# Kernel optimization log

Measured on AMD Instinct MI355X. Metric: run time of the kernel, lower is better.

## Reference

```python
import jax, jax.numpy as jnp
import numpy as np

B, C, H, W = 8, 512, 32, 32
N_HEADS = 4
D_K = C // N_HEADS  # 128


def setup_inputs() -> dict:
    key = jax.random.key(0)
    k1, k2, k3, k4, k5 = jax.random.split(key, 5)
    x = jax.random.normal(k1, (B, C, H, W), dtype=jnp.float32)
    # projection: Linear(in_ch, n_heads*d_k*3)
    Wp = jax.random.normal(k2, (C, N_HEADS * D_K * 3), dtype=jnp.float32) * (C ** -0.5)
    bp = jax.random.normal(k3, (N_HEADS * D_K * 3,), dtype=jnp.float32) * 0.01
    # output: Linear(n_heads*d_k, in_ch)
    Wo = jax.random.normal(k4, (N_HEADS * D_K, C), dtype=jnp.float32) * ((N_HEADS * D_K) ** -0.5)
    bo = jax.random.normal(k5, (C,), dtype=jnp.float32) * 0.01
    return {"x": x, "Wp": Wp, "bp": bp, "Wo": Wo, "bo": bo}


def reference(x, Wp, bp, Wo, bo):
    b, c, h, w = x.shape
    scale = D_K ** -0.5
    # [B, C, H, W] -> [B, N, C], N = H*W
    xs = x.reshape(b, c, h * w).transpose(0, 2, 1)
    qkv = (xs @ Wp + bp).reshape(b, h * w, N_HEADS, 3 * D_K)
    q, k, v = jnp.split(qkv, 3, axis=-1)  # each [B, N, H, D]
    attn = jnp.einsum('bihd,bjhd->bijh', q, k) * scale
    attn = jax.nn.softmax(attn, axis=2)  # softmax over j (keys)
    out = jnp.einsum('bijh,bjhd->bihd', attn, v)
    out = out.reshape(b, h * w, N_HEADS * D_K)
    out = out @ Wo + bo
    out = out + xs  # residual (note: GroupNorm is unused in the original forward)
    return out.transpose(0, 2, 1).reshape(b, c, h, w)
```

## Files before the change

### kernel.cpp

```cpp
#include <hip/hip_runtime.h>

#define NB 8
#define NC 512
#define NTOK 1024
#define NHEADS 4
#define DKH 128

typedef unsigned short u16;
typedef __attribute__((ext_vector_type(8))) short bf16x8;
typedef __attribute__((ext_vector_type(4))) float f32x4;

__device__ inline u16 f2b(float f) {
    union { float f; unsigned u; } v; v.f = f;
    unsigned r = v.u + 0x7fffu + ((v.u >> 16) & 1u);
    return (u16)(r >> 16);
}

__device__ __forceinline__ void gll16(const u16* g, u16* l) {
    __builtin_amdgcn_global_load_lds((const __attribute__((address_space(1))) unsigned*)g,
                                     (__attribute__((address_space(3))) unsigned*)l, 16, 0, 0);
}

__global__ __launch_bounds__(256) void prep(const float* __restrict__ x, const float* __restrict__ Wp,
                                            const float* __restrict__ Wo,
                                            u16* __restrict__ xsb, u16* __restrict__ WpT, u16* __restrict__ WoT)
{
    __shared__ float tile[32][33];
    const int z = blockIdx.z;
    const float* src; u16* dst; int R, Cc;
    if (z == 0)      { src = Wp; dst = WpT; R = 512; Cc = 1536; }
    else if (z == 1) { if (blockIdx.x >= 16) return; src = Wo; dst = WoT; R = 512; Cc = 512; }
    else             { if (blockIdx.x >= 32) return;
                       src = x + (long)(z-2)*NC*NTOK; dst = xsb + (long)(z-2)*NTOK*NC; R = NC; Cc = NTOK; }
    int c0 = blockIdx.x * 32, r0 = blockIdx.y * 32;
    int tx = threadIdx.x, ty = threadIdx.y;
    #pragma unroll
    for (int k = 0; k < 4; ++k)
        tile[ty + 8*k][tx] = src[(long)(r0 + ty + 8*k) * Cc + c0 + tx];
    __syncthreads();
    #pragma unroll
    for (int k = 0; k < 4; ++k)
        dst[(long)(c0 + ty + 8*k) * R + r0 + tx] = f2b(tile[tx][ty + 8*k]);
}

__global__ __launch_bounds__(512, 2) void gemm_qkv(const u16* __restrict__ WpT, const u16* __restrict__ xsb,
                                                   const float* __restrict__ bp,
                                                   u16* __restrict__ qg, u16* __restrict__ kg, u16* __restrict__ vg)
{
    __shared__ union SmU {
        struct { u16 As[2][256][64]; u16 Bs[2][256][64]; } s;
        u16 Os[8][64][72];
    } sm;
    const int tid = threadIdx.x;
    const int raw = blockIdx.x;
    const int L = (raw & 7) * 24 + (raw >> 3);
    const int mb = L % 6, nb = L / 6;
    const int m0 = mb * 256;
    const int n0 = nb * 256;
    const int w = tid >> 6, lane = tid & 63, quad = lane >> 4, lc = lane & 15;
    const int mo = (w & 1) * 128, no = (w >> 1) * 64;
    const int sw8 = (((lane & 7) ^ (lane >> 3)) << 3);
    const int xs = lc & 15 & 7;
    const int srow = (lane >> 3);

    f32x4 acc[8][4] = {};

    #pragma unroll
    for (int p = 0; p < 4; ++p) {
        int row = w*32 + p*8 + srow;
        gll16(&WpT[(long)(m0 + row) * NC + 0 + sw8], &sm.s.As[0][w*32 + p*8][0]);
        gll16(&xsb[(long)(n0 + row) * NC + 0 + sw8], &sm.s.Bs[0][w*32 + p*8][0]);
    }

    for (int t = 0; t < 8; ++t) {
        if (t < 7) {
            const long kk = (long)(t + 1) * 64;
            const int nbuf = (t + 1) & 1;
            #pragma unroll
            for (int p = 0; p < 4; ++p) {
                int row = w*32 + p*8 + srow;
                gll16(&WpT[(long)(m0 + row) * NC + kk + sw8], &sm.s.As[nbuf][w*32 + p*8][0]);
                gll16(&xsb[(long)(n0 + row) * NC + kk + sw8], &sm.s.Bs[nbuf][w*32 + p*8][0]);
            }
            asm volatile("s_waitcnt vmcnt(8)" ::: "memory");
        } else {
            asm volatile("s_waitcnt vmcnt(0)" ::: "memory");
        }
        __builtin_amdgcn_s_barrier();
        __builtin_amdgcn_sched_barrier(0);

        const int cb = t & 1;
        #pragma unroll
        for (int ks = 0; ks < 2; ++ks) {
            bf16x8 af[8], bfr[4];
            #pragma unroll
            for (int mt = 0; mt < 8; ++mt)
                af[mt] = *(const bf16x8*)&sm.s.As[cb][mo + mt*16 + lc][((ks*4 + quad) ^ xs) << 3];
            #pragma unroll
            for (int nt = 0; nt < 4; ++nt)
                bfr[nt] = *(const bf16x8*)&sm.s.Bs[cb][no + nt*16 + lc][((ks*4 + quad) ^ xs) << 3];
            __builtin_amdgcn_s_setprio(1);
            #pragma unroll
            for (int mt = 0; mt < 8; ++mt)
                #pragma unroll
                for (int nt = 0; nt < 4; ++nt)
                    acc[mt][nt] = __builtin_amdgcn_mfma_f32_16x16x32_bf16(af[mt], bfr[nt], acc[mt][nt], 0, 0, 0);
            __builtin_amdgcn_s_setprio(0);
        }
        __builtin_amdgcn_s_barrier();
    }

    const int bb = n0 >> 10;
    const int nblk = n0 & 1023;
    const int pb = (m0 + mo) >> 7;
    const int h = pb / 3;
    const int sel = pb % 3;
    const long bhbase = (long)(bb * NHEADS + h);

    #pragma unroll
    for (int mh = 0; mh < 2; ++mh) {
        const int d0 = mh * 64;
        #pragma unroll
        for (int mt4 = 0; mt4 < 4; ++mt4) {
            int mt = mh*4 + mt4;
            int cq0 = m0 + mo + mt*16 + quad*4;
            float b0 = bp[cq0+0], b1 = bp[cq0+1], b2 = bp[cq0+2], b3 = bp[cq0+3];
            #pragma unroll
            for (int nt = 0; nt < 4; ++nt) {
                f32x4 a = acc[mt][nt];
                int nl = nt*16 + lc;
                int ml = mt4*16 + quad*4;
                u16 e0 = f2b(a[0]+b0), e1 = f2b(a[1]+b1), e2 = f2b(a[2]+b2), e3 = f2b(a[3]+b3);
                if (sel == 2) {
                    sm.Os[w][ml+0][nl] = e0; sm.Os[w][ml+1][nl] = e1;
                    sm.Os[w][ml+2][nl] = e2; sm.Os[w][ml+3][nl] = e3;
                } else {
                    sm.Os[w][nl][ml+0] = e0; sm.Os[w][nl][ml+1] = e1;
                    sm.Os[w][nl][ml+2] = e2; sm.Os[w][nl][ml+3] = e3;
                }
            }
        }
        __builtin_amdgcn_sched_barrier(0);

        if (sel == 2) {
            #pragma unroll
            for (int pass = 0; pass < 8; ++pass) {
                int ml  = pass*8 + srow;
                int nl0 = (lane & 7) * 8;
                bf16x8 vv = *(const bf16x8*)&sm.Os[w][ml][nl0];
                *(bf16x8*)&vg[((bhbase*DKH + d0 + ml) << 10) + nblk + no + sw8] = vv;
            }
        } else if (sel == 1) {
            #pragma unroll
            for (int pass = 0; pass < 8; ++pass) {
                int nl  = pass*8 + srow;
                int ml0 = (lane & 7) * 8;
                bf16x8 vv = *(const bf16x8*)&sm.Os[w][nl][ml0];
                *(bf16x8*)&kg[((bhbase*NTOK + nblk + no + nl) << 7) + d0 + sw8] = vv;
            }
        } else {
            #pragma unroll
            for (int pass = 0; pass < 8; ++pass) {
                int nl  = pass*8 + srow;
                int ml0 = (lane & 7) * 8;
                bf16x8 vv = *(const bf16x8*)&sm.Os[w][nl][ml0];
                *(bf16x8*)&qg[((bhbase*NTOK + nblk + no + nl) << 7) + d0 + ml0] = vv;
            }
        }
        __builtin_amdgcn_sched_barrier(0);
    }
}

__global__ __launch_bounds__(512) void attn(const u16* __restrict__ qg, const u16* __restrict__ kg,
                                            const u16* __restrict__ vtg, u16* __restrict__ ho)
{
    __shared__ u16 Ks[2][64*128];
    __shared__ u16 Vt[2][128*64];
    __shared__ u16 Ps[8][16][72];
    const int tid = threadIdx.x;
    const int w = tid >> 6, lane = tid & 63, quad = lane >> 4, lc = lane & 15;
    const int id = blockIdx.x;
    const int xcd = id & 7, rest = id >> 3, sub = rest & 3, bx = rest >> 2;
    const int pr = xcd + sub*8;
    const int b = pr >> 2, h = pr & 3;
    const int i0 = bx*128 + w*16;
    const long bh = (long)(b * NHEADS + h) << 17;
    const u16* qb = qg + bh;
    const u16* kb = kg + bh;
    const u16* vb = vtg + bh;
    const float SL2E = 0.08838834764831845f * 1.4426950408889634f;

    bf16x8 qf[4];
    #pragma unroll
    for (int ks = 0; ks < 4; ++ks)
        qf[ks] = *(const bf16x8*)&qb[(long)(i0 + lc) * DKH + ks*32 + quad*8];

    f32x4 o[8] = {};
    float lsum = 0.f;
    const int xs = lc & 7;

    #pragma unroll
    for (int p = 0; p < 2; ++p) {
        int ck = (w*2 + p)*64 + lane;
        gll16(&kb[(long)ck * 8], &Ks[0][(w*2 + p)*512]);
        gll16(&vb[(((long)(ck >> 3)) << 10) + (ck & 7)*8], &Vt[0][(w*2 + p)*512]);
    }

    for (int t = 0; t < 16; ++t) {
        __syncthreads();
        if (t < 15) {
            long jo = (long)(t+1) * 64;
            #pragma unroll
            for (int p = 0; p < 2; ++p) {
                int ck = (w*2 + p)*64 + lane;
                gll16(&kb[jo*128 + (long)ck*8], &Ks[(t+1)&1][(w*2 + p)*512]);
                gll16(&vb[(((long)(ck >> 3)) << 10) + jo + (ck & 7)*8], &Vt[(t+1)&1][(w*2 + p)*512]);
            }
        }
        const u16* K = Ks[t&1];
        const u16* V = Vt[t&1];

        f32x4 s[4] = {};
        #pragma unroll
        for (int ks = 0; ks < 4; ++ks)
            #pragma unroll
            for (int jt = 0; jt < 4; ++jt) {
                bf16x8 kf = *(const bf16x8*)&K[(jt*16 + lc)*128 + (((ks*4 + quad) ^ xs) << 3)];
                s[jt] = __builtin_amdgcn_mfma_f32_16x16x32_bf16(kf, qf[ks], s[jt], 0, 0, 0);
            }

        #pragma unroll
        for (int jt = 0; jt < 4; ++jt) {
            float p0 = __builtin_amdgcn_exp2f(s[jt][0] * SL2E);
            float p1 = __builtin_amdgcn_exp2f(s[jt][1] * SL2E);
            float p2 = __builtin_amdgcn_exp2f(s[jt][2] * SL2E);
            float p3 = __builtin_amdgcn_exp2f(s[jt][3] * SL2E);
            lsum += (p0 + p1) + (p2 + p3);
            ushort4 pk;
            pk.x = f2b(p0); pk.y = f2b(p1); pk.z = f2b(p2); pk.w = f2b(p3);
            *(ushort4*)&Ps[w][lc][jt*16 + quad*4] = pk;
        }
        __builtin_amdgcn_sched_barrier(0);

        #pragma unroll
        for (int ks2 = 0; ks2 < 2; ++ks2) {
            bf16x8 pf = *(const bf16x8*)&Ps[w][lc][ks2*32 + quad*8];
            #pragma unroll
            for (int dt = 0; dt < 8; ++dt) {
                bf16x8 vf = *(const bf16x8*)&V[(dt*16 + lc)*64 + (((ks2*4 + quad) ^ xs) << 3)];
                o[dt] = __builtin_amdgcn_mfma_f32_16x16x32_bf16(vf, pf, o[dt], 0, 0, 0);
            }
        }
    }

    lsum += __shfl_xor(lsum, 16);
    lsum += __shfl_xor(lsum, 32);
    float inv = 1.0f / lsum;

    #pragma unroll
    for (int dt = 0; dt < 8; ++dt) {
        ushort4 pk;
        pk.x = f2b(o[dt][0] * inv); pk.y = f2b(o[dt][1] * inv);
        pk.z = f2b(o[dt][2] * inv); pk.w = f2b(o[dt][3] * inv);
        *(ushort4*)&ho[(long)(b*NTOK + i0 + lc) * NC + h*DKH + dt*16 + quad*4] = pk;
    }
}

__global__ __launch_bounds__(256) void gemm_out(const u16* __restrict__ WoT, const u16* __restrict__ ho,
                                                const float* __restrict__ bo, const float* __restrict__ xin,
                                                float* __restrict__ dout)
{
    __shared__ struct { u16 As[128][64]; u16 Bs[64][64]; } sm;
    const int tid = threadIdx.x;
    const int m0 = blockIdx.x * 128;
    const int n0 = blockIdx.y * 64;
    const int w = tid >> 6, lane = tid & 63, quad = lane >> 4, lc = lane & 15;
    const int mo = (w & 1) * 64, no = (w >> 1) * 32;
    const int sw8 = (((lane & 7) ^ (lane >> 3)) << 3);
    const int xs = lc & 7;

    f32x4 acc[4][2] = {};

    for (int k0 = 0; k0 < NC; k0 += 64) {
        __syncthreads();
        #pragma unroll
        for (int p = 0; p < 4; ++p) {
            int row = w*32 + p*8 + (lane >> 3);
            gll16(&WoT[(long)(m0 + row) * NC + k0 + sw8], &sm.As[w*32 + p*8][0]);
        }
        #pragma unroll
        for (int p = 0; p < 2; ++p) {
            int row = w*16 + p*8 + (lane >> 3);
            gll16(&ho[(long)(n0 + row) * NC + k0 + sw8], &sm.Bs[w*16 + p*8][0]);
        }
        __syncthreads();
        #pragma unroll
        for (int ks = 0; ks < 2; ++ks) {
            bf16x8 af[4], bfr[2];
            #pragma unroll
            for (int t = 0; t < 4; ++t)
                af[t] = *(const bf16x8*)&sm.As[mo + t*16 + lc][((ks*4 + quad) ^ xs) << 3];
            #pragma unroll
            for (int t = 0; t < 2; ++t)
                bfr[t] = *(const bf16x8*)&sm.Bs[no + t*16 + lc][((ks*4 + quad) ^ xs) << 3];
            #pragma unroll
            for (int mt = 0; mt < 4; ++mt)
                #pragma unroll
                for (int nt = 0; nt < 2; ++nt)
                    acc[mt][nt] = __builtin_amdgcn_mfma_f32_16x16x32_bf16(af[mt], bfr[nt], acc[mt][nt], 0, 0, 0);
        }
    }

    const int bb = n0 >> 10;
    #pragma unroll
    for (int mt = 0; mt < 4; ++mt) {
        int cc0 = m0 + mo + mt*16 + quad*4;
        float b0 = bo[cc0+0], b1 = bo[cc0+1], b2 = bo[cc0+2], b3 = bo[cc0+3];
        #pragma unroll
        for (int nt = 0; nt < 2; ++nt) {
            int nl = (n0 + no + nt*16 + lc) & (NTOK - 1);
            f32x4 a = acc[mt][nt];
            long ix = ((long)(bb*NC + cc0) << 10) + nl;
            dout[ix]             = a[0] + b0 + xin[ix];
            dout[ix + (1 << 10)] = a[1] + b1 + xin[ix + (1 << 10)];
            dout[ix + (2 << 10)] = a[2] + b2 + xin[ix + (2 << 10)];
            dout[ix + (3 << 10)] = a[3] + b3 + xin[ix + (3 << 10)];
        }
    }
}

extern "C" void kernel_launch(void* const* d_in, const int* in_sizes, int n_in,
                              void* d_out, int out_size, void* d_ws, size_t ws_size,
                              hipStream_t stream)
{
    (void)in_sizes; (void)n_in; (void)out_size; (void)ws_size;
    const float* x  = (const float*)d_in[0];
    const float* Wp = (const float*)d_in[1];
    const float* bp = (const float*)d_in[2];
    const float* Wo = (const float*)d_in[3];
    const float* bo = (const float*)d_in[4];
    float* out = (float*)d_out;

    u16* ws  = (u16*)d_ws;
    u16* xsb = ws;
    u16* WpT = xsb + (long)NB * NTOK * NC;
    u16* WoT = WpT + 1536L * 512;
    u16* qg  = WoT + 512L * 512;
    u16* kg  = qg + (long)NB * NHEADS * NTOK * DKH;
    u16* vtg = kg + (long)NB * NHEADS * NTOK * DKH;
    u16* ho  = vtg + (long)NB * NHEADS * NTOK * DKH;

    prep<<<dim3(48, 16, 10), dim3(32, 8), 0, stream>>>(x, Wp, Wo, xsb, WpT, WoT);
    gemm_qkv<<<dim3(192), 512, 0, stream>>>(WpT, xsb, bp, qg, kg, vtg);
    attn<<<dim3(256), 512, 0, stream>>>(qg, kg, vtg, ho);
    gemm_out<<<dim3(NC/128, (NB*NTOK)/64), 256, 0, stream>>>(WoT, ho, bo, x, out);
}
```

Measured before the change: 141.5 us.

## Read K and V tiles straight from global memory in attention, drop LDS staging

The attention kernel no longer double-buffers K and V^T tiles in shared memory with global_load_lds and block barriers. Each wave now loads its K and V fragments directly from global memory into registers, relying on L2/cache reuse across the eight waves of a block. The launch bounds also request two blocks per CU now that shared memory use is smaller. This removes __syncthreads and LDS traffic, but every wave issues redundant global loads. The loads keep the XOR swizzle in their addresses, which looks consistent only if the producer kernels already write K and V^T in that swizzled layout.

```diff
diff --git a/kernel.cpp b/kernel.cpp
--- a/kernel.cpp
+++ b/kernel.cpp
@@ -60,7 +60,7 @@
     const int w = tid >> 6, lane = tid & 63, quad = lane >> 4, lc = lane & 15;
     const int mo = (w & 1) * 128, no = (w >> 1) * 64;
     const int sw8 = (((lane & 7) ^ (lane >> 3)) << 3);
-    const int xs = lc & 15 & 7;
+    const int xs = lc & 7;
     const int srow = (lane >> 3);
 
     f32x4 acc[8][4] = {};
@@ -171,11 +171,9 @@
     }
 }
 
-__global__ __launch_bounds__(512) void attn(const u16* __restrict__ qg, const u16* __restrict__ kg,
-                                            const u16* __restrict__ vtg, u16* __restrict__ ho)
-{
-    __shared__ u16 Ks[2][64*128];
-    __shared__ u16 Vt[2][128*64];
+__global__ __launch_bounds__(512, 2) void attn(const u16* __restrict__ qg, const u16* __restrict__ kg,
+                                               const u16* __restrict__ vtg, u16* __restrict__ ho)
+{
     __shared__ u16 Ps[8][16][72];
     const int tid = threadIdx.x;
     const int w = tid >> 6, lane = tid & 63, quad = lane >> 4, lc = lane & 15;
@@ -199,35 +197,24 @@
     float lsum = 0.f;
     const int xs = lc & 7;
 
-    #pragma unroll
-    for (int p = 0; p < 2; ++p) {
-        int ck = (w*2 + p)*64 + lane;
-        gll16(&kb[(long)ck * 8], &Ks[0][(w*2 + p)*512]);
-        gll16(&vb[(((long)(ck >> 3)) << 10) + (ck & 7)*8], &Vt[0][(w*2 + p)*512]);
-    }
-
+    #pragma unroll 2
     for (int t = 0; t < 16; ++t) {
-        __syncthreads();
-        if (t < 15) {
-            long jo = (long)(t+1) * 64;
-            #pragma unroll
-            for (int p = 0; p < 2; ++p) {
-                int ck = (w*2 + p)*64 + lane;
-                gll16(&kb[jo*128 + (long)ck*8], &Ks[(t+1)&1][(w*2 + p)*512]);
-                gll16(&vb[(((long)(ck >> 3)) << 10) + jo + (ck & 7)*8], &Vt[(t+1)&1][(w*2 + p)*512]);
-            }
-        }
-        const u16* K = Ks[t&1];
-        const u16* V = Vt[t&1];
+        const u16* Kt = kb + (long)t * 64 * 128;
+        const u16* Vt = vb + t * 64;
+
+        bf16x8 kf[16];
+        #pragma unroll
+        for (int ks = 0; ks < 4; ++ks)
+            #pragma unroll
+            for (int jt = 0; jt < 4; ++jt)
+                kf[ks*4 + jt] = *(const bf16x8*)&Kt[(jt*16 + lc)*128 + (((ks*4 + quad) ^ xs) << 3)];
 
         f32x4 s[4] = {};
         #pragma unroll
         for (int ks = 0; ks < 4; ++ks)
             #pragma unroll
-            for (int jt = 0; jt < 4; ++jt) {
-                bf16x8 kf = *(const bf16x8*)&K[(jt*16 + lc)*128 + (((ks*4 + quad) ^ xs) << 3)];
-                s[jt] = __builtin_amdgcn_mfma_f32_16x16x32_bf16(kf, qf[ks], s[jt], 0, 0, 0);
-            }
+            for (int jt = 0; jt < 4; ++jt)
+                s[jt] = __builtin_amdgcn_mfma_f32_16x16x32_bf16(kf[ks*4 + jt], qf[ks], s[jt], 0, 0, 0);
 
         #pragma unroll
         for (int jt = 0; jt < 4; ++jt) {
@@ -247,7 +234,7 @@
             bf16x8 pf = *(const bf16x8*)&Ps[w][lc][ks2*32 + quad*8];
             #pragma unroll
             for (int dt = 0; dt < 8; ++dt) {
-                bf16x8 vf = *(const bf16x8*)&V[(dt*16 + lc)*64 + (((ks2*4 + quad) ^ xs) << 3)];
+                bf16x8 vf = *(const bf16x8*)&Vt[((long)(dt*16 + lc) << 10) + (((ks2*4 + quad) ^ xs) << 3)];
                 o[dt] = __builtin_amdgcn_mfma_f32_16x16x32_bf16(vf, pf, o[dt], 0, 0, 0);
             }
         }
```

New measurement: 161.0 us. 1.14x slower.

## Split attention keys across two wave groups per block and merge partial outputs

Applied to the files above, without the earlier changes.

The attention kernel grows to 1024 threads, with two groups of 8 waves each covering half of the 1024 keys for the same 128 queries. Each group double-buffers K in its own LDS region and loads V per step into a single buffer, using an explicit vmcnt wait plus barrier. At the end, partial outputs and row sums are reduced through an LDS union area. This doubles the waves per CU while each wave runs only 8 key tiles, at the cost of more LDS, extra barriers and a final cross-group reduction.

```diff
diff --git a/kernel.cpp b/kernel.cpp
--- a/kernel.cpp
+++ b/kernel.cpp
@@ -60,7 +60,7 @@
     const int w = tid >> 6, lane = tid & 63, quad = lane >> 4, lc = lane & 15;
     const int mo = (w & 1) * 128, no = (w >> 1) * 64;
     const int sw8 = (((lane & 7) ^ (lane >> 3)) << 3);
-    const int xs = lc & 15 & 7;
+    const int xs = lc & 7;
     const int srow = (lane >> 3);
 
     f32x4 acc[8][4] = {};
@@ -171,19 +171,21 @@
     }
 }
 
-__global__ __launch_bounds__(512) void attn(const u16* __restrict__ qg, const u16* __restrict__ kg,
-                                            const u16* __restrict__ vtg, u16* __restrict__ ho)
-{
-    __shared__ u16 Ks[2][64*128];
-    __shared__ u16 Vt[2][128*64];
-    __shared__ u16 Ps[8][16][72];
+__global__ __launch_bounds__(1024, 4) void attn(const u16* __restrict__ qg, const u16* __restrict__ kg,
+                                                const u16* __restrict__ vtg, u16* __restrict__ ho)
+{
+    __shared__ union AS {
+        struct { u16 Ks[2][2][64*128]; u16 Vt[2][128*64]; u16 Ps[16][16][72]; } m;
+        struct { float Om[8][16][132]; float Lm[8][16]; } g;
+    } sm;
     const int tid = threadIdx.x;
     const int w = tid >> 6, lane = tid & 63, quad = lane >> 4, lc = lane & 15;
+    const int ig = w & 7, jh = w >> 3;
     const int id = blockIdx.x;
     const int xcd = id & 7, rest = id >> 3, sub = rest & 3, bx = rest >> 2;
     const int pr = xcd + sub*8;
     const int b = pr >> 2, h = pr & 3;
-    const int i0 = bx*128 + w*16;
+    const int i0 = bx*128 + ig*16;
     const long bh = (long)(b * NHEADS + h) << 17;
     const u16* qb = qg + bh;
     const u16* kb = kg + bh;
@@ -198,27 +200,33 @@
     f32x4 o[8] = {};
     float lsum = 0.f;
     const int xs = lc & 7;
+    const long jbase = (long)jh * 8;
 
     #pragma unroll
     for (int p = 0; p < 2; ++p) {
-        int ck = (w*2 + p)*64 + lane;
-        gll16(&kb[(long)ck * 8], &Ks[0][(w*2 + p)*512]);
-        gll16(&vb[(((long)(ck >> 3)) << 10) + (ck & 7)*8], &Vt[0][(w*2 + p)*512]);
-    }
-
-    for (int t = 0; t < 16; ++t) {
+        int ck = (ig*2 + p)*64 + lane;
+        gll16(&kb[jbase*64*128 + (long)ck*8], &sm.m.Ks[jh][0][(ig*2 + p)*512]);
+    }
+
+    for (int t = 0; t < 8; ++t) {
         __syncthreads();
-        if (t < 15) {
-            long jo = (long)(t+1) * 64;
+        const long jo = (jbase + t) * 64;
+        #pragma unroll
+        for (int p = 0; p < 2; ++p) {
+            int ck = (ig*2 + p)*64 + lane;
+            gll16(&vb[(((long)(ck >> 3)) << 10) + jo + (ck & 7)*8], &sm.m.Vt[jh][(ig*2 + p)*512]);
+        }
+        if (t < 7) {
+            const long jo2 = (jbase + t + 1) * 64;
             #pragma unroll
             for (int p = 0; p < 2; ++p) {
-                int ck = (w*2 + p)*64 + lane;
-                gll16(&kb[jo*128 + (long)ck*8], &Ks[(t+1)&1][(w*2 + p)*512]);
-                gll16(&vb[(((long)(ck >> 3)) << 10) + jo + (ck & 7)*8], &Vt[(t+1)&1][(w*2 + p)*512]);
-            }
-        }
-        const u16* K = Ks[t&1];
-        const u16* V = Vt[t&1];
+                int ck = (ig*2 + p)*64 + lane;
+                gll16(&kb[jo2*128 + (long)ck*8], &sm.m.Ks[jh][(t+1)&1][(ig*2 + p)*512]);
+            }
+        }
+        __builtin_amdgcn_sched_barrier(0);
+
+        const u16* K = sm.m.Ks[jh][t&1];
 
         f32x4 s[4] = {};
         #pragma unroll
@@ -238,13 +246,18 @@
             lsum += (p0 + p1) + (p2 + p3);
             ushort4 pk;
             pk.x = f2b(p0); pk.y = f2b(p1); pk.z = f2b(p2); pk.w = f2b(p3);
-            *(ushort4*)&Ps[w][lc][jt*16 + quad*4] = pk;
-        }
-        __builtin_amdgcn_sched_barrier(0);
-
+            *(ushort4*)&sm.m.Ps[w][lc][jt*16 + quad*4] = pk;
+        }
+        __builtin_amdgcn_sched_barrier(0);
+
+        if (t < 7) { asm volatile("s_waitcnt vmcnt(2)" ::: "memory"); }
+        else       { asm volatile("s_waitcnt vmcnt(0)" ::: "memory"); }
+        __builtin_amdgcn_s_barrier();
+
+        const u16* V = sm.m.Vt[jh];
         #pragma unroll
         for (int ks2 = 0; ks2 < 2; ++ks2) {
-            bf16x8 pf = *(const bf16x8*)&Ps[w][lc][ks2*32 + quad*8];
+            bf16x8 pf = *(const bf16x8*)&sm.m.Ps[w][lc][ks2*32 + quad*8];
             #pragma unroll
             for (int dt = 0; dt < 8; ++dt) {
                 bf16x8 vf = *(const bf16x8*)&V[(dt*16 + lc)*64 + (((ks2*4 + quad) ^ xs) << 3)];
@@ -255,14 +268,27 @@
 
     lsum += __shfl_xor(lsum, 16);
     lsum += __shfl_xor(lsum, 32);
-    float inv = 1.0f / lsum;
-
-    #pragma unroll
-    for (int dt = 0; dt < 8; ++dt) {
-        ushort4 pk;
-        pk.x = f2b(o[dt][0] * inv); pk.y = f2b(o[dt][1] * inv);
-        pk.z = f2b(o[dt][2] * inv); pk.w = f2b(o[dt][3] * inv);
-        *(ushort4*)&ho[(long)(b*NTOK + i0 + lc) * NC + h*DKH + dt*16 + quad*4] = pk;
+
+    __syncthreads();
+    if (jh == 1) {
+        #pragma unroll
+        for (int dt = 0; dt < 8; ++dt)
+            *(f32x4*)&sm.g.Om[ig][lc][dt*16 + quad*4] = o[dt];
+        if (quad == 0) sm.g.Lm[ig][lc] = lsum;
+    }
+    __syncthreads();
+    if (jh == 0) {
+        float lt = lsum + sm.g.Lm[ig][lc];
+        float inv = 1.0f / lt;
+        #pragma unroll
+        for (int dt = 0; dt < 8; ++dt) {
+            f32x4 part = *(const f32x4*)&sm.g.Om[ig][lc][dt*16 + quad*4];
+            f32x4 tot = o[dt] + part;
+            ushort4 pk;
+            pk.x = f2b(tot[0] * inv); pk.y = f2b(tot[1] * inv);
+            pk.z = f2b(tot[2] * inv); pk.w = f2b(tot[3] * inv);
+            *(ushort4*)&ho[(long)(b*NTOK + i0 + lc) * NC + h*DKH + dt*16 + quad*4] = pk;
+        }
     }
 }
 
@@ -352,6 +378,6 @@
 
     prep<<<dim3(48, 16, 10), dim3(32, 8), 0, stream>>>(x, Wp, Wo, xsb, WpT, WoT);
     gemm_qkv<<<dim3(192), 512, 0, stream>>>(WpT, xsb, bp, qg, kg, vtg);
-    attn<<<dim3(256), 512, 0, stream>>>(qg, kg, vtg, ho);
+    attn<<<dim3(256), 1024, 0, stream>>>(qg, kg, vtg, ho);
     gemm_out<<<dim3(NC/128, (NB*NTOK)/64), 256, 0, stream>>>(WoT, ho, bo, x, out);
 }
```

After: 139.5 us. No clear change (-1.5%).

## Software-pipeline attention so QK^T of the next tile overlaps PV of the previous

Applied to the files above, without the earlier changes.

The attention loop is restructured so that each iteration computes QK^T and the softmax probabilities for tile t while running the PV MFMAs for tile t-1. To make this safe, the V tile is triple-buffered and the P scratch is double-buffered, with explicit vmcnt waits and barriers in place of the plain __syncthreads. The intent is to hide exp/convert latency and LDS round-trips behind MFMA work. In exchange, LDS use per block grows and the loop now has a prologue and epilogue. A redundant mask in the QKV GEMM is also simplified.

```diff
diff --git a/kernel.cpp b/kernel.cpp
--- a/kernel.cpp
+++ b/kernel.cpp
@@ -60,7 +60,7 @@
     const int w = tid >> 6, lane = tid & 63, quad = lane >> 4, lc = lane & 15;
     const int mo = (w & 1) * 128, no = (w >> 1) * 64;
     const int sw8 = (((lane & 7) ^ (lane >> 3)) << 3);
-    const int xs = lc & 15 & 7;
+    const int xs = lc & 7;
     const int srow = (lane >> 3);
 
     f32x4 acc[8][4] = {};
@@ -175,8 +175,8 @@
                                             const u16* __restrict__ vtg, u16* __restrict__ ho)
 {
     __shared__ u16 Ks[2][64*128];
-    __shared__ u16 Vt[2][128*64];
-    __shared__ u16 Ps[8][16][72];
+    __shared__ u16 Vt[3][128*64];
+    __shared__ u16 Ps[2][8][16][72];
     const int tid = threadIdx.x;
     const int w = tid >> 6, lane = tid & 63, quad = lane >> 4, lc = lane & 15;
     const int id = blockIdx.x;
@@ -194,32 +194,27 @@
     #pragma unroll
     for (int ks = 0; ks < 4; ++ks)
         qf[ks] = *(const bf16x8*)&qb[(long)(i0 + lc) * DKH + ks*32 + quad*8];
+    __builtin_amdgcn_sched_barrier(0);
 
     f32x4 o[8] = {};
     float lsum = 0.f;
     const int xs = lc & 7;
 
     #pragma unroll
-    for (int p = 0; p < 2; ++p) {
-        int ck = (w*2 + p)*64 + lane;
-        gll16(&kb[(long)ck * 8], &Ks[0][(w*2 + p)*512]);
-        gll16(&vb[(((long)(ck >> 3)) << 10) + (ck & 7)*8], &Vt[0][(w*2 + p)*512]);
-    }
-
-    for (int t = 0; t < 16; ++t) {
-        __syncthreads();
-        if (t < 15) {
-            long jo = (long)(t+1) * 64;
-            #pragma unroll
-            for (int p = 0; p < 2; ++p) {
-                int ck = (w*2 + p)*64 + lane;
-                gll16(&kb[jo*128 + (long)ck*8], &Ks[(t+1)&1][(w*2 + p)*512]);
-                gll16(&vb[(((long)(ck >> 3)) << 10) + jo + (ck & 7)*8], &Vt[(t+1)&1][(w*2 + p)*512]);
-            }
-        }
-        const u16* K = Ks[t&1];
-        const u16* V = Vt[t&1];
-
+    for (int tt = 0; tt < 2; ++tt) {
+        #pragma unroll
+        for (int p = 0; p < 2; ++p) {
+            int ck = (w*2 + p)*64 + lane;
+            gll16(&kb[(long)tt*64*128 + (long)ck*8], &Ks[tt][(w*2 + p)*512]);
+            gll16(&vb[(((long)(ck >> 3)) << 10) + tt*64 + (ck & 7)*8], &Vt[tt][(w*2 + p)*512]);
+        }
+    }
+
+    asm volatile("s_waitcnt vmcnt(4)" ::: "memory");
+    __builtin_amdgcn_s_barrier();
+    __builtin_amdgcn_sched_barrier(0);
+    {
+        const u16* K = Ks[0];
         f32x4 s[4] = {};
         #pragma unroll
         for (int ks = 0; ks < 4; ++ks)
@@ -228,7 +223,6 @@
                 bf16x8 kf = *(const bf16x8*)&K[(jt*16 + lc)*128 + (((ks*4 + quad) ^ xs) << 3)];
                 s[jt] = __builtin_amdgcn_mfma_f32_16x16x32_bf16(kf, qf[ks], s[jt], 0, 0, 0);
             }
-
         #pragma unroll
         for (int jt = 0; jt < 4; ++jt) {
             float p0 = __builtin_amdgcn_exp2f(s[jt][0] * SL2E);
@@ -238,13 +232,71 @@
             lsum += (p0 + p1) + (p2 + p3);
             ushort4 pk;
             pk.x = f2b(p0); pk.y = f2b(p1); pk.z = f2b(p2); pk.w = f2b(p3);
-            *(ushort4*)&Ps[w][lc][jt*16 + quad*4] = pk;
-        }
+            *(ushort4*)&Ps[0][w][lc][jt*16 + quad*4] = pk;
+        }
+    }
+
+    int vst = 2, vpv = 0;
+    for (int t = 1; t < 16; ++t) {
+        asm volatile("s_waitcnt vmcnt(0)" ::: "memory");
+        __builtin_amdgcn_s_barrier();
         __builtin_amdgcn_sched_barrier(0);
-
+        if (t < 15) {
+            long jo = (long)(t + 1) * 64;
+            #pragma unroll
+            for (int p = 0; p < 2; ++p) {
+                int ck = (w*2 + p)*64 + lane;
+                gll16(&kb[jo*128 + (long)ck*8], &Ks[(t+1)&1][(w*2 + p)*512]);
+                gll16(&vb[(((long)(ck >> 3)) << 10) + jo + (ck & 7)*8], &Vt[vst][(w*2 + p)*512]);
+            }
+            __builtin_amdgcn_sched_barrier(0);
+        }
+
+        const u16* K = Ks[t&1];
+        f32x4 s[4] = {};
+        #pragma unroll
+        for (int ks = 0; ks < 4; ++ks)
+            #pragma unroll
+            for (int jt = 0; jt < 4; ++jt) {
+                bf16x8 kf = *(const bf16x8*)&K[(jt*16 + lc)*128 + (((ks*4 + quad) ^ xs) << 3)];
+                s[jt] = __builtin_amdgcn_mfma_f32_16x16x32_bf16(kf, qf[ks], s[jt], 0, 0, 0);
+            }
+
+        {
+            const u16* V = Vt[vpv];
+            const u16* Pp = &Ps[(t-1)&1][w][0][0];
+            #pragma unroll
+            for (int ks2 = 0; ks2 < 2; ++ks2) {
+                bf16x8 pf = *(const bf16x8*)&Pp[lc*72 + ks2*32 + quad*8];
+                #pragma unroll
+                for (int dt = 0; dt < 8; ++dt) {
+                    bf16x8 vf = *(const bf16x8*)&V[(dt*16 + lc)*64 + (((ks2*4 + quad) ^ xs) << 3)];
+                    o[dt] = __builtin_amdgcn_mfma_f32_16x16x32_bf16(vf, pf, o[dt], 0, 0, 0);
+                }
+            }
+        }
+
+        #pragma unroll
+        for (int jt = 0; jt < 4; ++jt) {
+            float p0 = __builtin_amdgcn_exp2f(s[jt][0] * SL2E);
+            float p1 = __builtin_amdgcn_exp2f(s[jt][1] * SL2E);
+            float p2 = __builtin_amdgcn_exp2f(s[jt][2] * SL2E);
+            float p3 = __builtin_amdgcn_exp2f(s[jt][3] * SL2E);
+            lsum += (p0 + p1) + (p2 + p3);
+            ushort4 pk;
+            pk.x = f2b(p0); pk.y = f2b(p1); pk.z = f2b(p2); pk.w = f2b(p3);
+            *(ushort4*)&Ps[t&1][w][lc][jt*16 + quad*4] = pk;
+        }
+
+        vst = (vst == 2) ? 0 : vst + 1;
+        vpv = (vpv == 2) ? 0 : vpv + 1;
+    }
+
+    {
+        const u16* V = Vt[0];
         #pragma unroll
         for (int ks2 = 0; ks2 < 2; ++ks2) {
-            bf16x8 pf = *(const bf16x8*)&Ps[w][lc][ks2*32 + quad*8];
+            bf16x8 pf = *(const bf16x8*)&Ps[1][w][lc][ks2*32 + quad*8];
             #pragma unroll
             for (int dt = 0; dt < 8; ++dt) {
                 bf16x8 vf = *(const bf16x8*)&V[(dt*16 + lc)*64 + (((ks2*4 + quad) ^ xs) << 3)];
```

New measurement: 140.5 us. No clear change (-0.8%).
